# Performance work log

Hardware: AMD Instinct MI355X
Metric: run time of the kernel (lower is better)

Reference implementation:

```python
import jax, jax.numpy as jnp
import numpy as np

T, B, IN, H, OUT = 128, 128, 512, 512, 512


def _lstm_dir(x, W_ih, W_hh, b_ih, b_hh):
    # x: [T, B, IN]; W_ih: [4H, IN]; W_hh: [4H, H]; biases: [4H]
    # Precompute input contribution for all timesteps in one big GEMM.
    xw = jnp.einsum('tbi,gi->tbg', x, W_ih) + b_ih + b_hh  # [T, B, 4H]
    Hh = W_hh.shape[1]

    def step(carry, xw_t):
        h, c = carry
        gates = xw_t + h @ W_hh.T  # [B, 4H]
        i, f, g, o = jnp.split(gates, 4, axis=-1)  # PyTorch gate order i,f,g,o
        i = jax.nn.sigmoid(i)
        f = jax.nn.sigmoid(f)
        g = jnp.tanh(g)
        o = jax.nn.sigmoid(o)
        c = f * c + i * g
        h = o * jnp.tanh(c)
        return (h, c), h

    h0 = jnp.zeros((x.shape[1], Hh), x.dtype)
    c0 = jnp.zeros((x.shape[1], Hh), x.dtype)
    _, hs = jax.lax.scan(step, (h0, c0), xw)
    return hs  # [T, B, H]


def setup_inputs() -> dict:
    key = jax.random.key(0)
    ks = jax.random.split(key, 12)
    s_in = 1.0 / np.sqrt(H)
    u = lambda k, shape: jax.random.uniform(k, shape, jnp.float32, -s_in, s_in)
    return {
        'x': jax.random.normal(ks[0], (T, B, IN), jnp.float32),
        'W_ih_f': u(ks[1], (4 * H, IN)),
        'W_hh_f': u(ks[2], (4 * H, H)),
        'b_ih_f': u(ks[3], (4 * H,)),
        'b_hh_f': u(ks[4], (4 * H,)),
        'W_ih_b': u(ks[5], (4 * H, IN)),
        'W_hh_b': u(ks[6], (4 * H, H)),
        'b_ih_b': u(ks[7], (4 * H,)),
        'b_hh_b': u(ks[8], (4 * H,)),
        'W_lin': u(ks[9], (OUT, 2 * H)),
        'b_lin': u(ks[10], (OUT,)),
    }


def reference(x, W_ih_f, W_hh_f, b_ih_f, b_hh_f, W_ih_b, W_hh_b, b_ih_b, b_hh_b, W_lin, b_lin):
    h_fwd = _lstm_dir(x, W_ih_f, W_hh_f, b_ih_f, b_hh_f)                    # [T,B,H]
    h_bwd = _lstm_dir(x[::-1], W_ih_b, W_hh_b, b_ih_b, b_hh_b)[::-1]        # [T,B,H]
    out = jnp.concatenate([h_fwd, h_bwd], axis=-1)                          # [T,B,2H]
    out = jnp.einsum('tbh,oh->tbo', out, W_lin) + b_lin                     # [T,B,OUT]
    return out
```

## Files before the change

kernel.cpp:

```cpp
#include <hip/hip_runtime.h>

typedef unsigned short u16;
typedef unsigned long long u64;
typedef __attribute__((ext_vector_type(8))) short bf16x8;
typedef __attribute__((ext_vector_type(4))) float f32x4;

#define MFMA16(a, b, c) __builtin_amdgcn_mfma_f32_16x16x32_bf16((a), (b), (c), 0, 0, 0)

#define TT 128
#define BB 128
#define IN_ 512
#define HH 512
#define G4 2048
#define OUTD 512
#define TB 16384

__device__ __forceinline__ u16 f2bf(float f) {
    union { float f; unsigned u; } v; v.f = f;
    unsigned r = v.u + 0x7FFFu + ((v.u >> 16) & 1u);
    return (u16)(r >> 16);
}
__device__ __forceinline__ float bf2f(u16 h) {
    union { unsigned u; float f; } v; v.u = ((unsigned)h) << 16; return v.f;
}
__device__ __forceinline__ float sigmoid_f(float x) { return 1.f / (1.f + __expf(-x)); }
__device__ __forceinline__ float tanh_f(float x) {
    float e = __expf(2.f * x);
    return 1.f - 2.f / (e + 1.f);
}

__global__ void cvt_kernel(const float* __restrict__ src, u16* __restrict__ dst, int n4) {
    int i = blockIdx.x * blockDim.x + threadIdx.x;
    int stride = gridDim.x * blockDim.x;
    for (; i < n4; i += stride) {
        float4 v = ((const float4*)src)[i];
        ushort4 o;
        o.x = f2bf(v.x); o.y = f2bf(v.y); o.z = f2bf(v.z); o.w = f2bf(v.w);
        ((ushort4*)dst)[i] = o;
    }
}

__global__ void bias_kernel(const float* __restrict__ bihf, const float* __restrict__ bhhf,
                            float* __restrict__ bf_, const float* __restrict__ bihb,
                            const float* __restrict__ bhhb, float* __restrict__ bb_, int n) {
    int i = blockIdx.x * blockDim.x + threadIdx.x;
    if (i < n) {
        bf_[i] = bihf[i] + bhhf[i];
        bb_[i] = bihb[i] + bhhb[i];
    }
}

__global__ void zero_exch_kernel(uint4* __restrict__ p) {
    int i = blockIdx.x * blockDim.x + threadIdx.x;
    p[i] = uint4{0u, 0u, 0u, 0u};
}

__global__ __launch_bounds__(256) void gemm_bias_kernel(
    const u16* __restrict__ A, const u16* __restrict__ W,
    const float* __restrict__ bias, void* __restrict__ Cout,
    int M, int N, int K, int out_is_bf16) {
    __shared__ __align__(16) u16 lA[128 * 72];
    __shared__ __align__(16) u16 lB[128 * 72];
    const int tid = threadIdx.x;
    const int m0 = blockIdx.x * 128;
    const int n0 = blockIdx.y * 128;
    const int wave = tid >> 6, lane = tid & 63;
    const int wm = wave >> 1, wn = wave & 1;
    const int lrow = lane & 15, lq = lane >> 4;

    f32x4 acc[4][4] = {};

    for (int kc = 0; kc < K; kc += 64) {
        #pragma unroll
        for (int i = 0; i < 4; ++i) {
            int c = i * 256 + tid;
            int row = c >> 3, off = c & 7;
            *(uint4*)(&lA[row * 72 + off * 8]) =
                *(const uint4*)(&A[(size_t)(m0 + row) * K + kc + off * 8]);
            *(uint4*)(&lB[row * 72 + off * 8]) =
                *(const uint4*)(&W[(size_t)(n0 + row) * K + kc + off * 8]);
        }
        __syncthreads();
        #pragma unroll
        for (int ks = 0; ks < 2; ++ks) {
            bf16x8 af[4], bfr[4];
            #pragma unroll
            for (int mf = 0; mf < 4; ++mf)
                af[mf] = *(const bf16x8*)(&lA[(wm * 64 + mf * 16 + lrow) * 72 + ks * 32 + lq * 8]);
            #pragma unroll
            for (int nf = 0; nf < 4; ++nf)
                bfr[nf] = *(const bf16x8*)(&lB[(wn * 64 + nf * 16 + lrow) * 72 + ks * 32 + lq * 8]);
            #pragma unroll
            for (int mf = 0; mf < 4; ++mf)
                #pragma unroll
                for (int nf = 0; nf < 4; ++nf)
                    acc[mf][nf] = MFMA16(af[mf], bfr[nf], acc[mf][nf]);
        }
        __syncthreads();
    }

    #pragma unroll
    for (int mf = 0; mf < 4; ++mf) {
        #pragma unroll
        for (int nf = 0; nf < 4; ++nf) {
            int row = m0 + wm * 64 + mf * 16 + lq * 4;
            int col = n0 + wn * 64 + nf * 16 + lrow;
            float bv = bias[col];
            f32x4 v = acc[mf][nf];
            #pragma unroll
            for (int r = 0; r < 4; ++r) {
                float val = v[r] + bv;
                if (out_is_bf16)
                    ((u16*)Cout)[(size_t)(row + r) * N + col] = f2bf(val);
                else
                    ((float*)Cout)[(size_t)(row + r) * N + col] = val;
            }
        }
    }
}

__global__ __launch_bounds__(256, 1) void lstm_persist_kernel(
    const u16* __restrict__ xw_f, const u16* __restrict__ xw_b,
    const u16* __restrict__ whh_f, const u16* __restrict__ whh_b,
    u16* __restrict__ hcat, u64* __restrict__ exch) {
    const int bx = blockIdx.x;
    const int dir = bx >> 7;
    const int bt = (bx >> 4) & 7;
    const int jt = bx & 15;
    const u16* __restrict__ xw  = dir ? xw_b : xw_f;
    const u16* __restrict__ whh = dir ? whh_b : whh_f;
    const int b0 = bt * 16;
    const int j0 = jt * 32;

    __shared__ __align__(16) u16 lh[16 * 520];
    __shared__ float sgate[4][16][33];

    const int tid = threadIdx.x;
    const int wave = tid >> 6, lane = tid & 63;
    const int lrow = lane & 15, lq = lane >> 4;

    const u16* wrow = whh + ((size_t)wave * HH + j0) * HH;
    bf16x8 w0[16], w1[16];
    #pragma unroll
    for (int kc = 0; kc < 16; ++kc) {
        w0[kc] = *(const bf16x8*)(&wrow[(size_t)lrow * HH + kc * 32 + lq * 8]);
        w1[kc] = *(const bf16x8*)(&wrow[(size_t)(16 + lrow) * HH + kc * 32 + lq * 8]);
    }
    #pragma unroll
    for (int kc = 0; kc < 16; ++kc)
        asm volatile("" : "+v"(w0[kc]), "+v"(w1[kc]));

    const int bl = tid >> 4;
    const int jj = (tid & 15) * 2;
    float cr0 = 0.f, cr1 = 0.f;

    const size_t my_ex = ((size_t)(dir)*BB + b0 + bl) * 256 + (j0 >> 1) + (tid & 15);

    for (int s = 0; s < TT; ++s) {
        const int t = dir ? (TT - 1 - s) : s;

        const u16* xrow = xw + ((size_t)t * BB + b0 + bl) * G4 + j0 + jj;
        unsigned xg[4];
        #pragma unroll
        for (int g = 0; g < 4; ++g)
            xg[g] = *(const unsigned*)(xrow + (size_t)g * HH);

        f32x4 acc0 = {}, acc1 = {}, acc0b = {}, acc1b = {};
        if (s > 0) {
            const int p = (s - 1) & 1;
            const u64* ex = exch + ((size_t)(p * 2 + dir) * BB + b0) * 256 + tid;
            const u64 expect = ((u64)(unsigned)s << 48) | ((u64)(unsigned)s << 16);
            u64 v[16];
            for (;;) {
                #pragma unroll
                for (int i = 0; i < 16; ++i)
                    v[i] = __hip_atomic_load(ex + (size_t)i * 256,
                                             __ATOMIC_RELAXED, __HIP_MEMORY_SCOPE_AGENT);
                bool ok = true;
                #pragma unroll
                for (int i = 0; i < 16; ++i)
                    ok &= ((v[i] & 0xFFFF0000FFFF0000ull) == expect);
                if (ok) break;
            }
            #pragma unroll
            for (int i = 0; i < 16; ++i)
                *(unsigned*)(&lh[i * 520 + tid * 2]) =
                    (unsigned)(v[i] & 0xffffu) | (unsigned)((v[i] >> 16) & 0xffff0000u);
            __syncthreads();

            #pragma unroll
            for (int kc = 0; kc < 16; kc += 2) {
                bf16x8 a0 = *(const bf16x8*)(&lh[lrow * 520 + kc * 32 + lq * 8]);
                bf16x8 a1 = *(const bf16x8*)(&lh[lrow * 520 + (kc + 1) * 32 + lq * 8]);
                acc0  = MFMA16(a0, w0[kc], acc0);
                acc1  = MFMA16(a0, w1[kc], acc1);
                acc0b = MFMA16(a1, w0[kc + 1], acc0b);
                acc1b = MFMA16(a1, w1[kc + 1], acc1b);
            }
            acc0 += acc0b;
            acc1 += acc1b;
        }

        #pragma unroll
        for (int r = 0; r < 4; ++r) {
            sgate[wave][lq * 4 + r][lrow]      = acc0[r];
            sgate[wave][lq * 4 + r][16 + lrow] = acc1[r];
        }
        __syncthreads();

        float gi0 = sgate[0][bl][jj]     + bf2f((u16)(xg[0] & 0xffffu));
        float gf0 = sgate[1][bl][jj]     + bf2f((u16)(xg[1] & 0xffffu));
        float gg0 = sgate[2][bl][jj]     + bf2f((u16)(xg[2] & 0xffffu));
        float go0 = sgate[3][bl][jj]     + bf2f((u16)(xg[3] & 0xffffu));
        float gi1 = sgate[0][bl][jj + 1] + bf2f((u16)(xg[0] >> 16));
        float gf1 = sgate[1][bl][jj + 1] + bf2f((u16)(xg[1] >> 16));
        float gg1 = sgate[2][bl][jj + 1] + bf2f((u16)(xg[2] >> 16));
        float go1 = sgate[3][bl][jj + 1] + bf2f((u16)(xg[3] >> 16));

        float c0 = sigmoid_f(gf0) * cr0 + sigmoid_f(gi0) * tanh_f(gg0);
        float c1 = sigmoid_f(gf1) * cr1 + sigmoid_f(gi1) * tanh_f(gg1);
        cr0 = c0; cr1 = c1;
        float h0 = sigmoid_f(go0) * tanh_f(c0);
        float h1 = sigmoid_f(go1) * tanh_f(c1);

        unsigned hb0 = (unsigned)f2bf(h0), hb1 = (unsigned)f2bf(h1);
        unsigned tagv = (unsigned)(s + 1) << 16;
        u64 pv = (u64)(tagv | hb0) | ((u64)(tagv | hb1) << 32);
        __hip_atomic_store(exch + (size_t)((s & 1) * 2) * BB * 256 + my_ex, pv,
                           __ATOMIC_RELAXED, __HIP_MEMORY_SCOPE_AGENT);

        *(unsigned*)(hcat + ((size_t)t * BB + b0 + bl) * (2 * HH) + dir * HH + j0 + jj) =
            hb0 | (hb1 << 16);
    }
}

#define OFF_XBF    ((size_t)0)
#define OFF_WIHF   (OFF_XBF  + (size_t)TB * IN_ * 2)
#define OFF_WIHB   (OFF_WIHF + (size_t)G4 * IN_ * 2)
#define OFF_WHHF   (OFF_WIHB + (size_t)G4 * IN_ * 2)
#define OFF_WHHB   (OFF_WHHF + (size_t)G4 * HH * 2)
#define OFF_WLIN   (OFF_WHHB + (size_t)G4 * HH * 2)
#define OFF_BIASF  (OFF_WLIN + (size_t)OUTD * 2 * HH * 2)
#define OFF_BIASB  (OFF_BIASF + (size_t)G4 * 4)
#define OFF_XWF    (OFF_BIASB + (size_t)G4 * 4)
#define OFF_XWB    (OFF_XWF  + (size_t)TB * G4 * 2)
#define OFF_HCAT   (OFF_XWB  + (size_t)TB * G4 * 2)
#define OFF_EXCH   (OFF_HCAT + (size_t)TB * 2 * HH * 2)
#define WS_NEED    (OFF_EXCH + (size_t)2 * 2 * BB * HH * 4)

extern "C" void kernel_launch(void* const* d_in, const int* in_sizes, int n_in,
                              void* d_out, int out_size, void* d_ws, size_t ws_size,
                              hipStream_t stream) {
    (void)in_sizes; (void)n_in; (void)out_size;
    if (ws_size < WS_NEED) return;

    const float* x    = (const float*)d_in[0];
    const float* Wihf = (const float*)d_in[1];
    const float* Whhf = (const float*)d_in[2];
    const float* bihf = (const float*)d_in[3];
    const float* bhhf = (const float*)d_in[4];
    const float* Wihb = (const float*)d_in[5];
    const float* Whhb = (const float*)d_in[6];
    const float* bihb = (const float*)d_in[7];
    const float* bhhb = (const float*)d_in[8];
    const float* Wlin = (const float*)d_in[9];
    const float* blin = (const float*)d_in[10];
    float* out = (float*)d_out;

    char* ws = (char*)d_ws;
    u16* x_bf    = (u16*)(ws + OFF_XBF);
    u16* wihf_bf = (u16*)(ws + OFF_WIHF);
    u16* wihb_bf = (u16*)(ws + OFF_WIHB);
    u16* whhf_bf = (u16*)(ws + OFF_WHHF);
    u16* whhb_bf = (u16*)(ws + OFF_WHHB);
    u16* wlin_bf = (u16*)(ws + OFF_WLIN);
    float* bias_f = (float*)(ws + OFF_BIASF);
    float* bias_b = (float*)(ws + OFF_BIASB);
    u16* xw_f = (u16*)(ws + OFF_XWF);
    u16* xw_b = (u16*)(ws + OFF_XWB);
    u16* hcat = (u16*)(ws + OFF_HCAT);
    u64* exch = (u64*)(ws + OFF_EXCH);

    cvt_kernel<<<2048, 256, 0, stream>>>(x, x_bf, (TB * IN_) / 4);
    cvt_kernel<<<512, 256, 0, stream>>>(Wihf, wihf_bf, (G4 * IN_) / 4);
    cvt_kernel<<<512, 256, 0, stream>>>(Wihb, wihb_bf, (G4 * IN_) / 4);
    cvt_kernel<<<512, 256, 0, stream>>>(Whhf, whhf_bf, (G4 * HH) / 4);
    cvt_kernel<<<512, 256, 0, stream>>>(Whhb, whhb_bf, (G4 * HH) / 4);
    cvt_kernel<<<512, 256, 0, stream>>>(Wlin, wlin_bf, (OUTD * 2 * HH) / 4);
    bias_kernel<<<8, 256, 0, stream>>>(bihf, bhhf, bias_f, bihb, bhhb, bias_b, G4);
    zero_exch_kernel<<<256, 256, 0, stream>>>((uint4*)exch);

    gemm_bias_kernel<<<dim3(TB / 128, G4 / 128), 256, 0, stream>>>(
        x_bf, wihf_bf, bias_f, xw_f, TB, G4, IN_, 1);
    gemm_bias_kernel<<<dim3(TB / 128, G4 / 128), 256, 0, stream>>>(
        x_bf, wihb_bf, bias_b, xw_b, TB, G4, IN_, 1);

    {
        void* args[] = { (void*)&xw_f, (void*)&xw_b, (void*)&whhf_bf, (void*)&whhb_bf,
                         (void*)&hcat, (void*)&exch };
        hipError_t e = hipLaunchCooperativeKernel(
            (const void*)lstm_persist_kernel, dim3(256), dim3(256), args, 0, stream);
        if (e != hipSuccess) {
            lstm_persist_kernel<<<256, 256, 0, stream>>>(xw_f, xw_b, whhf_bf, whhb_bf,
                                                         hcat, exch);
        }
    }

    gemm_bias_kernel<<<dim3(TB / 128, OUTD / 128), 256, 0, stream>>>(
        hcat, wlin_bf, blin, out, TB, OUTD, 2 * HH, 0);
}
```

Baseline: 698.1 us.

## Fuse prep kernels, merge direction GEMMs, and use global_load_lds in GEMM

The eight conversion, bias and zeroing launches become one grid-stride prep kernel. The two input-projection GEMMs become one GEMM over concatenated weights, with the LSTM reading an interleaved xw layout. The GEMM tile loads now use global_load_lds direct-to-LDS transfers with an unpadded 64-wide LDS row. This cuts launch overhead and register staging, but the unpadded LDS rows may cause bank conflicts on fragment reads.

```diff
diff --git a/kernel.cpp b/kernel.cpp
--- a/kernel.cpp
+++ b/kernel.cpp
@@ -15,6 +15,8 @@
 #define OUTD 512
 #define TB 16384
 
+#define AEXLD(p) __hip_atomic_load((p), __ATOMIC_RELAXED, __HIP_MEMORY_SCOPE_AGENT)
+
 __device__ __forceinline__ u16 f2bf(float f) {
     union { float f; unsigned u; } v; v.f = f;
     unsigned r = v.u + 0x7FFFu + ((v.u >> 16) & 1u);
@@ -29,56 +31,71 @@
     return 1.f - 2.f / (e + 1.f);
 }
 
-__global__ void cvt_kernel(const float* __restrict__ src, u16* __restrict__ dst, int n4) {
-    int i = blockIdx.x * blockDim.x + threadIdx.x;
-    int stride = gridDim.x * blockDim.x;
-    for (; i < n4; i += stride) {
-        float4 v = ((const float4*)src)[i];
-        ushort4 o;
-        o.x = f2bf(v.x); o.y = f2bf(v.y); o.z = f2bf(v.z); o.w = f2bf(v.w);
-        ((ushort4*)dst)[i] = o;
-    }
-}
-
-__global__ void bias_kernel(const float* __restrict__ bihf, const float* __restrict__ bhhf,
-                            float* __restrict__ bf_, const float* __restrict__ bihb,
-                            const float* __restrict__ bhhb, float* __restrict__ bb_, int n) {
-    int i = blockIdx.x * blockDim.x + threadIdx.x;
-    if (i < n) {
-        bf_[i] = bihf[i] + bhhf[i];
-        bb_[i] = bihb[i] + bhhb[i];
-    }
-}
-
-__global__ void zero_exch_kernel(uint4* __restrict__ p) {
-    int i = blockIdx.x * blockDim.x + threadIdx.x;
-    p[i] = uint4{0u, 0u, 0u, 0u};
+typedef unsigned __attribute__((address_space(1))) guint;
+typedef unsigned __attribute__((address_space(3))) luint;
+__device__ __forceinline__ void gll16(const u16* g, u16* l) {
+    __builtin_amdgcn_global_load_lds((guint*)(void*)g, (luint*)(void*)l, 16, 0, 0);
+}
+
+__global__ void prep_kernel(
+    const float* __restrict__ x,
+    const float* __restrict__ Wihf, const float* __restrict__ Wihb,
+    const float* __restrict__ Whhf, const float* __restrict__ Whhb,
+    const float* __restrict__ Wlin,
+    const float* __restrict__ bihf, const float* __restrict__ bhhf,
+    const float* __restrict__ bihb, const float* __restrict__ bhhb,
+    u16* __restrict__ x_bf, u16* __restrict__ wih_cat,
+    u16* __restrict__ whhf_bf, u16* __restrict__ whhb_bf,
+    u16* __restrict__ wlin_bf, float* __restrict__ bias_cat,
+    uint4* __restrict__ exch) {
+    const int i0 = blockIdx.x * blockDim.x + threadIdx.x;
+    const int stride = gridDim.x * blockDim.x;
+    #define CVT4(SRC, DST, N4, DOFF)                                        \
+        for (int i = i0; i < (N4); i += stride) {                           \
+            float4 v = ((const float4*)(SRC))[i];                           \
+            ushort4 o;                                                      \
+            o.x = f2bf(v.x); o.y = f2bf(v.y);                               \
+            o.z = f2bf(v.z); o.w = f2bf(v.w);                               \
+            ((ushort4*)(DST))[(DOFF) + i] = o;                              \
+        }
+    CVT4(x, x_bf, (TB * IN_) / 4, 0)
+    CVT4(Wihf, wih_cat, (G4 * IN_) / 4, 0)
+    CVT4(Wihb, wih_cat, (G4 * IN_) / 4, (G4 * IN_) / 4)
+    CVT4(Whhf, whhf_bf, (G4 * HH) / 4, 0)
+    CVT4(Whhb, whhb_bf, (G4 * HH) / 4, 0)
+    CVT4(Wlin, wlin_bf, (OUTD * 2 * HH) / 4, 0)
+    #undef CVT4
+    for (int i = i0; i < G4; i += stride) {
+        bias_cat[i]      = bihf[i] + bhhf[i];
+        bias_cat[G4 + i] = bihb[i] + bhhb[i];
+    }
+    for (int i = i0; i < 65536; i += stride)
+        exch[i] = uint4{0u, 0u, 0u, 0u};
 }
 
 __global__ __launch_bounds__(256) void gemm_bias_kernel(
     const u16* __restrict__ A, const u16* __restrict__ W,
     const float* __restrict__ bias, void* __restrict__ Cout,
     int M, int N, int K, int out_is_bf16) {
-    __shared__ __align__(16) u16 lA[128 * 72];
-    __shared__ __align__(16) u16 lB[128 * 72];
+    __shared__ __align__(16) u16 lA[128 * 64];
+    __shared__ __align__(16) u16 lB[128 * 64];
     const int tid = threadIdx.x;
     const int m0 = blockIdx.x * 128;
     const int n0 = blockIdx.y * 128;
     const int wave = tid >> 6, lane = tid & 63;
     const int wm = wave >> 1, wn = wave & 1;
     const int lrow = lane & 15, lq = lane >> 4;
+    const int srow = lane >> 3, soff = (lane & 7) * 8;
 
     f32x4 acc[4][4] = {};
 
     for (int kc = 0; kc < K; kc += 64) {
         #pragma unroll
         for (int i = 0; i < 4; ++i) {
-            int c = i * 256 + tid;
-            int row = c >> 3, off = c & 7;
-            *(uint4*)(&lA[row * 72 + off * 8]) =
-                *(const uint4*)(&A[(size_t)(m0 + row) * K + kc + off * 8]);
-            *(uint4*)(&lB[row * 72 + off * 8]) =
-                *(const uint4*)(&W[(size_t)(n0 + row) * K + kc + off * 8]);
+            int chunk = wave + i * 4;
+            int row = chunk * 8 + srow;
+            gll16(&A[(size_t)(m0 + row) * K + kc + soff], &lA[chunk * 512]);
+            gll16(&W[(size_t)(n0 + row) * K + kc + soff], &lB[chunk * 512]);
         }
         __syncthreads();
         #pragma unroll
@@ -86,10 +103,10 @@
             bf16x8 af[4], bfr[4];
             #pragma unroll
             for (int mf = 0; mf < 4; ++mf)
-                af[mf] = *(const bf16x8*)(&lA[(wm * 64 + mf * 16 + lrow) * 72 + ks * 32 + lq * 8]);
+                af[mf] = *(const bf16x8*)(&lA[(wm * 64 + mf * 16 + lrow) * 64 + ks * 32 + lq * 8]);
             #pragma unroll
             for (int nf = 0; nf < 4; ++nf)
-                bfr[nf] = *(const bf16x8*)(&lB[(wn * 64 + nf * 16 + lrow) * 72 + ks * 32 + lq * 8]);
+                bfr[nf] = *(const bf16x8*)(&lB[(wn * 64 + nf * 16 + lrow) * 64 + ks * 32 + lq * 8]);
             #pragma unroll
             for (int mf = 0; mf < 4; ++mf)
                 #pragma unroll
@@ -120,14 +137,13 @@
 }
 
 __global__ __launch_bounds__(256, 1) void lstm_persist_kernel(
-    const u16* __restrict__ xw_f, const u16* __restrict__ xw_b,
-    const u16* __restrict__ whh_f, const u16* __restrict__ whh_b,
-    u16* __restrict__ hcat, u64* __restrict__ exch) {
+    const u16* __restrict__ xw, const u16* __restrict__ whh_f,
+    const u16* __restrict__ whh_b, u16* __restrict__ hcat,
+    u64* __restrict__ exch) {
     const int bx = blockIdx.x;
     const int dir = bx >> 7;
     const int bt = (bx >> 4) & 7;
     const int jt = bx & 15;
-    const u16* __restrict__ xw  = dir ? xw_b : xw_f;
     const u16* __restrict__ whh = dir ? whh_b : whh_f;
     const int b0 = bt * 16;
     const int j0 = jt * 32;
@@ -154,12 +170,12 @@
     const int jj = (tid & 15) * 2;
     float cr0 = 0.f, cr1 = 0.f;
 
-    const size_t my_ex = ((size_t)(dir)*BB + b0 + bl) * 256 + (j0 >> 1) + (tid & 15);
+    const size_t my_ex = ((size_t)dir * BB + b0 + bl) * 256 + (j0 >> 1) + (tid & 15);
 
     for (int s = 0; s < TT; ++s) {
         const int t = dir ? (TT - 1 - s) : s;
 
-        const u16* xrow = xw + ((size_t)t * BB + b0 + bl) * G4 + j0 + jj;
+        const u16* xrow = xw + ((size_t)t * BB + b0 + bl) * (2 * G4) + dir * G4 + j0 + jj;
         unsigned xg[4];
         #pragma unroll
         for (int g = 0; g < 4; ++g)
@@ -174,8 +190,7 @@
             for (;;) {
                 #pragma unroll
                 for (int i = 0; i < 16; ++i)
-                    v[i] = __hip_atomic_load(ex + (size_t)i * 256,
-                                             __ATOMIC_RELAXED, __HIP_MEMORY_SCOPE_AGENT);
+                    v[i] = AEXLD(ex + (size_t)i * 256);
                 bool ok = true;
                 #pragma unroll
                 for (int i = 0; i < 16; ++i)
@@ -235,16 +250,13 @@
 }
 
 #define OFF_XBF    ((size_t)0)
-#define OFF_WIHF   (OFF_XBF  + (size_t)TB * IN_ * 2)
-#define OFF_WIHB   (OFF_WIHF + (size_t)G4 * IN_ * 2)
-#define OFF_WHHF   (OFF_WIHB + (size_t)G4 * IN_ * 2)
+#define OFF_WIH    (OFF_XBF  + (size_t)TB * IN_ * 2)
+#define OFF_WHHF   (OFF_WIH  + (size_t)2 * G4 * IN_ * 2)
 #define OFF_WHHB   (OFF_WHHF + (size_t)G4 * HH * 2)
 #define OFF_WLIN   (OFF_WHHB + (size_t)G4 * HH * 2)
-#define OFF_BIASF  (OFF_WLIN + (size_t)OUTD * 2 * HH * 2)
-#define OFF_BIASB  (OFF_BIASF + (size_t)G4 * 4)
-#define OFF_XWF    (OFF_BIASB + (size_t)G4 * 4)
-#define OFF_XWB    (OFF_XWF  + (size_t)TB * G4 * 2)
-#define OFF_HCAT   (OFF_XWB  + (size_t)TB * G4 * 2)
+#define OFF_BIAS   (OFF_WLIN + (size_t)OUTD * 2 * HH * 2)
+#define OFF_XW     (OFF_BIAS + (size_t)2 * G4 * 4)
+#define OFF_HCAT   (OFF_XW   + (size_t)TB * 2 * G4 * 2)
 #define OFF_EXCH   (OFF_HCAT + (size_t)TB * 2 * HH * 2)
 #define WS_NEED    (OFF_EXCH + (size_t)2 * 2 * BB * HH * 4)
 
@@ -268,40 +280,31 @@
     float* out = (float*)d_out;
 
     char* ws = (char*)d_ws;
-    u16* x_bf    = (u16*)(ws + OFF_XBF);
-    u16* wihf_bf = (u16*)(ws + OFF_WIHF);
-    u16* wihb_bf = (u16*)(ws + OFF_WIHB);
-    u16* whhf_bf = (u16*)(ws + OFF_WHHF);
-    u16* whhb_bf = (u16*)(ws + OFF_WHHB);
-    u16* wlin_bf = (u16*)(ws + OFF_WLIN);
-    float* bias_f = (float*)(ws + OFF_BIASF);
-    float* bias_b = (float*)(ws + OFF_BIASB);
-    u16* xw_f = (u16*)(ws + OFF_XWF);
-    u16* xw_b = (u16*)(ws + OFF_XWB);
+    u16* x_bf     = (u16*)(ws + OFF_XBF);
+    u16* wih_cat  = (u16*)(ws + OFF_WIH);
+    u16* whhf_bf  = (u16*)(ws + OFF_WHHF);
+    u16* whhb_bf  = (u16*)(ws + OFF_WHHB);
+    u16* wlin_bf  = (u16*)(ws + OFF_WLIN);
+    float* bias_cat = (float*)(ws + OFF_BIAS);
+    u16* xw   = (u16*)(ws + OFF_XW);
     u16* hcat = (u16*)(ws + OFF_HCAT);
     u64* exch = (u64*)(ws + OFF_EXCH);
 
-    cvt_kernel<<<2048, 256, 0, stream>>>(x, x_bf, (TB * IN_) / 4);
-    cvt_kernel<<<512, 256, 0, stream>>>(Wihf, wihf_bf, (G4 * IN_) / 4);
-    cvt_kernel<<<512, 256, 0, stream>>>(Wihb, wihb_bf, (G4 * IN_) / 4);
-    cvt_kernel<<<512, 256, 0, stream>>>(Whhf, whhf_bf, (G4 * HH) / 4);
-    cvt_kernel<<<512, 256, 0, stream>>>(Whhb, whhb_bf, (G4 * HH) / 4);
-    cvt_kernel<<<512, 256, 0, stream>>>(Wlin, wlin_bf, (OUTD * 2 * HH) / 4);
-    bias_kernel<<<8, 256, 0, stream>>>(bihf, bhhf, bias_f, bihb, bhhb, bias_b, G4);
-    zero_exch_kernel<<<256, 256, 0, stream>>>((uint4*)exch);
-
-    gemm_bias_kernel<<<dim3(TB / 128, G4 / 128), 256, 0, stream>>>(
-        x_bf, wihf_bf, bias_f, xw_f, TB, G4, IN_, 1);
-    gemm_bias_kernel<<<dim3(TB / 128, G4 / 128), 256, 0, stream>>>(
-        x_bf, wihb_bf, bias_b, xw_b, TB, G4, IN_, 1);
+    prep_kernel<<<1024, 256, 0, stream>>>(x, Wihf, Wihb, Whhf, Whhb, Wlin,
+                                          bihf, bhhf, bihb, bhhb,
+                                          x_bf, wih_cat, whhf_bf, whhb_bf, wlin_bf,
+                                          bias_cat, (uint4*)exch);
+
+    gemm_bias_kernel<<<dim3(TB / 128, (2 * G4) / 128), 256, 0, stream>>>(
+        x_bf, wih_cat, bias_cat, xw, TB, 2 * G4, IN_, 1);
 
     {
-        void* args[] = { (void*)&xw_f, (void*)&xw_b, (void*)&whhf_bf, (void*)&whhb_bf,
+        void* args[] = { (void*)&xw, (void*)&whhf_bf, (void*)&whhb_bf,
                          (void*)&hcat, (void*)&exch };
         hipError_t e = hipLaunchCooperativeKernel(
             (const void*)lstm_persist_kernel, dim3(256), dim3(256), args, 0, stream);
         if (e != hipSuccess) {
-            lstm_persist_kernel<<<256, 256, 0, stream>>>(xw_f, xw_b, whhf_bf, whhb_bf,
+            lstm_persist_kernel<<<256, 256, 0, stream>>>(xw, whhf_bf, whhb_bf,
                                                          hcat, exch);
         }
     }
```

Result: no change. 693.1 us (-0.7%).
